# Kernel optimization log

Measured on AMD Instinct MI355X. Metric: run time of the kernel, lower is better.

The kernel has to match this reference:

```python
import jax, jax.numpy as jnp
import numpy as np

H3, W3, D3 = 12, 12, 12
NUM_HEADS = 8
DIM = 128
BATCH = 4
N_TOK = H3 * W3 * D3  # 1728
TABLE = (2 * H3 - 1) * (2 * W3 - 1) * (2 * D3 - 1)  # 12167


def _relative_position_index(h, w, d):
    ch, cw, cd = np.arange(h), np.arange(w), np.arange(d)
    coords = np.stack(np.meshgrid(ch, cw, cd, indexing='ij'))  # (3,h,w,d)
    cf = coords.reshape(3, -1)  # (3,N)
    rel = cf[:, :, None] - cf[:, None, :]  # (3,N,N)
    rel = rel.transpose(1, 2, 0).copy()
    rel[:, :, 0] += h - 1
    rel[:, :, 1] += w - 1
    rel[:, :, 2] += d - 1
    rel[:, :, 0] *= (2 * w - 1) * (2 * d - 1)
    rel[:, :, 1] *= 2 * d - 1
    return rel.sum(-1).astype(np.int32)  # (N,N)


def setup_inputs() -> dict:
    key = jax.random.key(0)
    ks = jax.random.split(key, 7)
    s = 1.0 / np.sqrt(DIM)
    return {
        'x': jax.random.normal(ks[0], (BATCH, N_TOK, DIM), jnp.float32),
        'Wq': jax.random.normal(ks[1], (DIM, DIM), jnp.float32) * s,
        'Wk': jax.random.normal(ks[2], (DIM, DIM), jnp.float32) * s,
        'Wv': jax.random.normal(ks[3], (DIM, DIM), jnp.float32) * s,
        'Wp': jax.random.normal(ks[4], (DIM, DIM), jnp.float32) * s,
        'bp': jnp.zeros((DIM,), jnp.float32),
        'rel_pos_table': jax.random.normal(ks[5], (TABLE, NUM_HEADS), jnp.float32) * 0.02,
        'rel_index': jnp.asarray(_relative_position_index(H3, W3, D3)),
    }


def reference(x, Wq, Wk, Wv, Wp, bp, rel_pos_table, rel_index):
    B, N, C = x.shape
    H = NUM_HEADS
    hd = C // H
    # projections (qkv_bias=False), split heads -> (B,H,N,hd)
    q = (x @ Wq.T).reshape(B, N, H, hd).transpose(0, 2, 1, 3)
    k = (x @ Wk.T).reshape(B, N, H, hd).transpose(0, 2, 1, 3)
    v = (x @ Wv.T).reshape(B, N, H, hd).transpose(0, 2, 1, 3)
    q_sig = jax.nn.sigmoid(q)
    # relative position bias: (N,N,H) -> (H,N,N)
    bias = rel_pos_table[rel_index.reshape(-1)].reshape(N, N, H).transpose(2, 0, 1)
    # softmax over key dim j of (k[b,h,j,d] + bias[h,i,j]) is separable:
    #   exp(k_jd + b_ij) = exp(b_ij - bmax_i) * exp(k_jd - kmax_d) * const
    kmax = jnp.max(k, axis=2, keepdims=True)            # (B,H,1,hd)
    bmax = jnp.max(bias, axis=2, keepdims=True)         # (H,N,1)
    ek = jnp.exp(k - kmax)                              # (B,H,N,hd)
    eb = jnp.exp(bias - bmax)                           # (H,N,N)
    num = jnp.einsum('hij,bhjd->bhid', eb, ek * v)      # (B,H,N,hd)
    den = jnp.einsum('hij,bhjd->bhid', eb, ek)          # (B,H,N,hd)
    out = q_sig * (num / den)                           # (B,H,N,hd)
    out = out.transpose(0, 2, 1, 3).reshape(B, N, C)
    return out @ Wp.T + bp
```

## Files before the change

kernel.cpp:

```cpp
#include <hip/hip_runtime.h>
#include <hip/hip_bf16.h>
#include <cmath>

#define NTOK 1728
#define DIMC 128
#define NHEAD 8
#define NB 4
#define TABN (12167 * 8)

typedef __attribute__((ext_vector_type(8))) short bf16x8;
typedef __attribute__((ext_vector_type(4))) float f32x4;

static __device__ __forceinline__ unsigned short f2bf(float f) {
    union { float f; unsigned u; } v; v.f = f;
    unsigned r = v.u + 0x7fff + ((v.u >> 16) & 1);
    return (unsigned short)(r >> 16);
}

__global__ __launch_bounds__(256) void k_proj_qkv(
    const float* __restrict__ x, const float* __restrict__ Wq,
    const float* __restrict__ Wk, const float* __restrict__ Wv,
    const float* __restrict__ tbl, unsigned short* __restrict__ tblm1,
    float* __restrict__ QS, float* __restrict__ Ko, float* __restrict__ Vo)
{
    __shared__ __align__(16) float xs[64 * 128];
    __shared__ __align__(16) float Ws[32 * 128];
    const int t = threadIdx.x;
    const int m = blockIdx.z;
    if (m == 3) {
        const int g = (blockIdx.y * 108 + blockIdx.x) * 256 + t;
        if (g < TABN) tblm1[g] = f2bf(expm1f(tbl[g]));
        return;
    }
    const int row0 = blockIdx.x * 64;
    const int cg = blockIdx.y;
    const float* __restrict__ W = (m == 0) ? Wq : (m == 1) ? Wk : Wv;

    {
        const int cc = t & 31;
        #pragma unroll
        for (int p = 0; p < 8; ++p) {
            const int r = (t >> 5) + p * 8;
            float4 v = *reinterpret_cast<const float4*>(&x[(size_t)(row0 + r) * DIMC + cc * 4]);
            *reinterpret_cast<float4*>(&xs[r * 128 + ((cc * 4) ^ ((r & 7) << 2))]) = v;
        }
    }
    {
        const int cc = t & 31;
        #pragma unroll
        for (int p = 0; p < 4; ++p) {
            const int c = (t >> 5) + p * 8;
            float4 v = *reinterpret_cast<const float4*>(&W[(size_t)(cg * 32 + c) * DIMC + cc * 4]);
            *reinterpret_cast<float4*>(&Ws[c * 128 + cc * 4]) = v;
        }
    }
    __syncthreads();
    const int nl = t & 63, w = t >> 6;
    float acc[8];
    #pragma unroll
    for (int c = 0; c < 8; ++c) acc[c] = 0.f;
    for (int k4 = 0; k4 < 32; ++k4) {
        const float4 xv = *reinterpret_cast<const float4*>(
            &xs[nl * 128 + ((k4 * 4) ^ ((nl & 7) << 2))]);
        #pragma unroll
        for (int c = 0; c < 8; ++c) {
            const float4 wv = *reinterpret_cast<const float4*>(&Ws[(w * 8 + c) * 128 + k4 * 4]);
            acc[c] = fmaf(xv.x, wv.x, fmaf(xv.y, wv.y,
                     fmaf(xv.z, wv.z, fmaf(xv.w, wv.w, acc[c]))));
        }
    }
    if (m == 0) {
        #pragma unroll
        for (int c = 0; c < 8; ++c) acc[c] = 1.f / (1.f + expf(-acc[c]));
    }
    __syncthreads();
    float* res = Ws;
    #pragma unroll
    for (int c = 0; c < 8; ++c) res[nl * 33 + w * 8 + c] = acc[c];
    __syncthreads();
    float* __restrict__ Out = (m == 0) ? QS : (m == 1) ? Ko : Vo;
    {
        const int r = t >> 2, q = t & 3;
        float4 v0, v1;
        v0.x = res[r*33 + q*8 + 0]; v0.y = res[r*33 + q*8 + 1];
        v0.z = res[r*33 + q*8 + 2]; v0.w = res[r*33 + q*8 + 3];
        v1.x = res[r*33 + q*8 + 4]; v1.y = res[r*33 + q*8 + 5];
        v1.z = res[r*33 + q*8 + 6]; v1.w = res[r*33 + q*8 + 7];
        *reinterpret_cast<float4*>(&Out[(size_t)(row0 + r) * DIMC + cg * 32 + q * 8]) = v0;
        *reinterpret_cast<float4*>(&Out[(size_t)(row0 + r) * DIMC + cg * 32 + q * 8 + 4]) = v1;
    }
}

__global__ __launch_bounds__(256) void k_build_ekv(
    const float* __restrict__ Ko, const float* __restrict__ Vo,
    unsigned short* __restrict__ EKVt, float* __restrict__ n1)
{
    __shared__ float red[256][33];
    const int t = threadIdx.x;
    const int h = blockIdx.y;
    const int b = t >> 6, jj = t & 63;
    const int j = blockIdx.x * 64 + jj;
    const float* kp = &Ko[((size_t)b * NTOK + j) * DIMC + h * 16];
    const float* vp = &Vo[((size_t)b * NTOK + j) * DIMC + h * 16];
    float kv[16], vv[16], ob[32];
    #pragma unroll
    for (int d4 = 0; d4 < 4; ++d4) {
        *reinterpret_cast<float4*>(&kv[d4 * 4]) = *reinterpret_cast<const float4*>(&kp[d4 * 4]);
        *reinterpret_cast<float4*>(&vv[d4 * 4]) = *reinterpret_cast<const float4*>(&vp[d4 * 4]);
    }
    #pragma unroll
    for (int d = 0; d < 16; ++d) {
        float e = expf(kv[d]);
        ob[d] = e * vv[d];
        ob[16 + d] = e;
    }
    #pragma unroll
    for (int c = 0; c < 32; ++c)
        EKVt[((size_t)h * DIMC + b * 32 + c) * NTOK + j] = f2bf(ob[c]);
    #pragma unroll
    for (int c = 0; c < 32; ++c) red[t][c] = ob[c];
    __syncthreads();
    if (t < 128) {
        const int b2 = t >> 5, c = t & 31;
        float s = 0.f;
        for (int r = 0; r < 64; ++r) s += red[b2 * 64 + r][c];
        atomicAdd(&n1[(h * NB + b2) * 32 + c], s);
    }
}

__global__ __launch_bounds__(256) void k_aft_mfma(
    const unsigned short* __restrict__ tblm1,
    const unsigned short* __restrict__ EKVt,
    float* __restrict__ part)
{
    __shared__ __align__(16) unsigned short alds[64 * 64];
    __shared__ __align__(16) unsigned short blds[128 * 64];
    const int t = threadIdx.x;
    const int i0 = blockIdx.x * 64;
    const int h = blockIdx.y;
    const int js = blockIdx.z;
    const int l = t & 63, w = t >> 6;
    const int il = l & 15, kg = l >> 4;

    const int gj = l;
    const int gi0 = w * 16;
    unsigned qb[16];
    #pragma unroll
    for (int r = 0; r < 16; ++r) {
        const int i = i0 + gi0 + r;
        const int hi = i / 144, wi = (i / 12) % 12, di = i % 12;
        qb[r] = (unsigned)((hi * 529 + wi * 23 + di + 6083) * 8 + h);
    }
    const int bc = t >> 3;
    const int bj8 = (t & 7) * 8;

    f32x4 acc[8];
    #pragma unroll
    for (int cf = 0; cf < 8; ++cf) acc[cf] = (f32x4){0.f, 0.f, 0.f, 0.f};

    for (int jt = 0; jt < 9; ++jt) {
        const int j0 = (js * 9 + jt) * 64;
        const int j = j0 + gj;
        const int hj = j / 144, wj = (j / 12) % 12, dj = j % 12;
        const unsigned pj8 = (unsigned)((hj * 529 + wj * 23 + dj) * 8);
        __syncthreads();
        #pragma unroll
        for (int p = 0; p < 4; ++p) {
            const int c = bc + p * 32;
            bf16x8 v = *reinterpret_cast<const bf16x8*>(
                &EKVt[((size_t)h * DIMC + c) * NTOK + j0 + bj8]);
            *reinterpret_cast<bf16x8*>(&blds[c * 64 + (bj8 ^ ((c & 7) << 3))]) = v;
        }
        #pragma unroll
        for (int r = 0; r < 16; ++r) {
            const unsigned short wv = tblm1[qb[r] - pj8];
            alds[(gi0 + r) * 64 + (gj ^ ((r & 7) << 3))] = wv;
        }
        __syncthreads();
        #pragma unroll
        for (int kk = 0; kk < 2; ++kk) {
            const int ia = w * 16 + il;
            const int ka = kk * 32 + kg * 8;
            bf16x8 af = *reinterpret_cast<const bf16x8*>(
                &alds[ia * 64 + (ka ^ ((ia & 7) << 3))]);
            #pragma unroll
            for (int cf = 0; cf < 8; ++cf) {
                const int cb = cf * 16 + il;
                bf16x8 bf = *reinterpret_cast<const bf16x8*>(
                    &blds[cb * 64 + (ka ^ ((cb & 7) << 3))]);
                acc[cf] = __builtin_amdgcn_mfma_f32_16x16x32_bf16(af, bf, acc[cf], 0, 0, 0);
            }
        }
    }
    #pragma unroll
    for (int cf = 0; cf < 8; ++cf) {
        #pragma unroll
        for (int r = 0; r < 4; ++r) {
            const int i = i0 + w * 16 + kg * 4 + r;
            const int c = cf * 16 + il;
            part[(((size_t)js * NHEAD + h) * NTOK + i) * DIMC + c] = acc[cf][r];
        }
    }
}

__global__ __launch_bounds__(256) void k_reduce_y(
    const float* __restrict__ part, const float* __restrict__ n1,
    const float* __restrict__ QS, float* __restrict__ Y)
{
    const int gid = blockIdx.x * 256 + threadIdx.x;
    const int h = gid / (NB * NTOK);
    const int bi = gid - h * (NB * NTOK);
    const int b = bi / NTOK;
    const int i = bi - b * NTOK;
    float nu[16], de[16];
    const float* np = &n1[(h * NB + b) * 32];
    #pragma unroll
    for (int d = 0; d < 16; ++d) { nu[d] = np[d]; de[d] = np[16 + d]; }
    #pragma unroll
    for (int js = 0; js < 3; ++js) {
        const float* pp = &part[(((size_t)js * NHEAD + h) * NTOK + i) * DIMC + b * 32];
        #pragma unroll
        for (int c4 = 0; c4 < 4; ++c4) {
            float4 a  = *reinterpret_cast<const float4*>(&pp[c4 * 4]);
            float4 d4 = *reinterpret_cast<const float4*>(&pp[16 + c4 * 4]);
            nu[c4*4+0] += a.x;  nu[c4*4+1] += a.y;  nu[c4*4+2] += a.z;  nu[c4*4+3] += a.w;
            de[c4*4+0] += d4.x; de[c4*4+1] += d4.y; de[c4*4+2] += d4.z; de[c4*4+3] += d4.w;
        }
    }
    const size_t yb = ((size_t)b * NTOK + i) * DIMC + h * 16;
    #pragma unroll
    for (int d4 = 0; d4 < 4; ++d4) {
        float4 q4 = *reinterpret_cast<const float4*>(&QS[yb + d4 * 4]);
        float4 o;
        o.x = q4.x * nu[d4*4+0] / de[d4*4+0];
        o.y = q4.y * nu[d4*4+1] / de[d4*4+1];
        o.z = q4.z * nu[d4*4+2] / de[d4*4+2];
        o.w = q4.w * nu[d4*4+3] / de[d4*4+3];
        *reinterpret_cast<float4*>(&Y[yb + d4 * 4]) = o;
    }
}

__global__ __launch_bounds__(256) void k_proj_out(
    const float* __restrict__ Y, const float* __restrict__ Wp,
    const float* __restrict__ bp, float* __restrict__ out)
{
    __shared__ __align__(16) float xs[64 * 128];
    __shared__ __align__(16) float Ws[32 * 128];
    const int t = threadIdx.x;
    const int row0 = blockIdx.x * 64;
    const int cg = blockIdx.y;
    {
        const int cc = t & 31;
        #pragma unroll
        for (int p = 0; p < 8; ++p) {
            const int r = (t >> 5) + p * 8;
            float4 v = *reinterpret_cast<const float4*>(&Y[(size_t)(row0 + r) * DIMC + cc * 4]);
            *reinterpret_cast<float4*>(&xs[r * 128 + ((cc * 4) ^ ((r & 7) << 2))]) = v;
        }
    }
    {
        const int cc = t & 31;
        #pragma unroll
        for (int p = 0; p < 4; ++p) {
            const int c = (t >> 5) + p * 8;
            float4 v = *reinterpret_cast<const float4*>(&Wp[(size_t)(cg * 32 + c) * DIMC + cc * 4]);
            *reinterpret_cast<float4*>(&Ws[c * 128 + cc * 4]) = v;
        }
    }
    __syncthreads();
    const int nl = t & 63, w = t >> 6;
    float acc[8];
    #pragma unroll
    for (int c = 0; c < 8; ++c) acc[c] = 0.f;
    for (int k4 = 0; k4 < 32; ++k4) {
        const float4 xv = *reinterpret_cast<const float4*>(
            &xs[nl * 128 + ((k4 * 4) ^ ((nl & 7) << 2))]);
        #pragma unroll
        for (int c = 0; c < 8; ++c) {
            const float4 wv = *reinterpret_cast<const float4*>(&Ws[(w * 8 + c) * 128 + k4 * 4]);
            acc[c] = fmaf(xv.x, wv.x, fmaf(xv.y, wv.y,
                     fmaf(xv.z, wv.z, fmaf(xv.w, wv.w, acc[c]))));
        }
    }
    #pragma unroll
    for (int c = 0; c < 8; ++c) acc[c] += bp[cg * 32 + w * 8 + c];
    __syncthreads();
    float* res = Ws;
    #pragma unroll
    for (int c = 0; c < 8; ++c) res[nl * 33 + w * 8 + c] = acc[c];
    __syncthreads();
    {
        const int r = t >> 2, q = t & 3;
        float4 v0, v1;
        v0.x = res[r*33 + q*8 + 0]; v0.y = res[r*33 + q*8 + 1];
        v0.z = res[r*33 + q*8 + 2]; v0.w = res[r*33 + q*8 + 3];
        v1.x = res[r*33 + q*8 + 4]; v1.y = res[r*33 + q*8 + 5];
        v1.z = res[r*33 + q*8 + 6]; v1.w = res[r*33 + q*8 + 7];
        *reinterpret_cast<float4*>(&out[(size_t)(row0 + r) * DIMC + cg * 32 + q * 8]) = v0;
        *reinterpret_cast<float4*>(&out[(size_t)(row0 + r) * DIMC + cg * 32 + q * 8 + 4]) = v1;
    }
}

extern "C" void kernel_launch(void* const* d_in, const int* in_sizes, int n_in,
                              void* d_out, int out_size, void* d_ws, size_t ws_size,
                              hipStream_t stream) {
    const float* x    = (const float*)d_in[0];
    const float* Wq   = (const float*)d_in[1];
    const float* Wk   = (const float*)d_in[2];
    const float* Wv   = (const float*)d_in[3];
    const float* Wp   = (const float*)d_in[4];
    const float* bp   = (const float*)d_in[5];
    const float* tbl  = (const float*)d_in[6];
    float* out = (float*)d_out;

    float* ws = (float*)d_ws;
    unsigned short* tblm1 = (unsigned short*)ws;
    float* QS  = ws + 48672;
    float* Ko  = QS + 884736;
    float* Vo  = Ko + 884736;
    unsigned short* EKVt = (unsigned short*)(Vo + 884736);
    float* n1   = Vo + 884736 + 884736;
    float* part = n1 + 1024;
    float* Yb   = part + (size_t)3 * NHEAD * NTOK * DIMC;

    hipMemsetAsync(n1, 0, 1024 * sizeof(float), stream);
    k_proj_qkv<<<dim3(108, 4, 4), 256, 0, stream>>>(x, Wq, Wk, Wv, tbl, tblm1, QS, Ko, Vo);
    k_build_ekv<<<dim3(27, 8), 256, 0, stream>>>(Ko, Vo, EKVt, n1);
    k_aft_mfma<<<dim3(27, 8, 3), 256, 0, stream>>>(tblm1, EKVt, part);
    k_reduce_y<<<dim3(216), 256, 0, stream>>>(part, n1, QS, Yb);
    k_proj_out<<<dim3(108, 4), 256, 0, stream>>>(Yb, Wp, bp, out);
}
```

Before: 166.9 us.

## Transpose bias table per head, stage window in LDS, restructure partial reduction

The exp-bias table is now stored head-major, so each attention block loads a contiguous 2304-entry window of it into shared memory once. The per-tile gather then reads LDS instead of scattered global memory. The partials layout is changed so the reduce kernel reads contiguously with one float4 per thread, and the n1 memset is folded into the projection kernel, removing one launch. This adds some LDS use and depends on the index window bounds being correct.

```diff
diff --git a/kernel.cpp b/kernel.cpp
--- a/kernel.cpp
+++ b/kernel.cpp
@@ -6,7 +6,8 @@
 #define DIMC 128
 #define NHEAD 8
 #define NB 4
-#define TABN (12167 * 8)
+#define TABN 12167
+#define TSTRIDE 12168
 
 typedef __attribute__((ext_vector_type(8))) short bf16x8;
 typedef __attribute__((ext_vector_type(4))) float f32x4;
@@ -17,10 +18,15 @@
     return (unsigned short)(r >> 16);
 }
 
+static __device__ __forceinline__ int Pdec(int t) {
+    return (t / 144) * 529 + ((t / 12) % 12) * 23 + (t % 12);
+}
+
 __global__ __launch_bounds__(256) void k_proj_qkv(
     const float* __restrict__ x, const float* __restrict__ Wq,
     const float* __restrict__ Wk, const float* __restrict__ Wv,
-    const float* __restrict__ tbl, unsigned short* __restrict__ tblm1,
+    const float* __restrict__ tbl, unsigned short* __restrict__ tblT,
+    float* __restrict__ n1,
     float* __restrict__ QS, float* __restrict__ Ko, float* __restrict__ Vo)
 {
     __shared__ __align__(16) float xs[64 * 128];
@@ -28,8 +34,24 @@
     const int t = threadIdx.x;
     const int m = blockIdx.z;
     if (m == 3) {
-        const int g = (blockIdx.y * 108 + blockIdx.x) * 256 + t;
-        if (g < TABN) tblm1[g] = f2bf(expm1f(tbl[g]));
+        const int bid2 = blockIdx.y * 108 + blockIdx.x;
+        if (bid2 < 48) {
+            const int idx = bid2 * 256 + t;
+            if (idx < TABN) {
+                float4 f0 = *reinterpret_cast<const float4*>(&tbl[idx * 8]);
+                float4 f1 = *reinterpret_cast<const float4*>(&tbl[idx * 8 + 4]);
+                tblT[0 * TSTRIDE + idx] = f2bf(expm1f(f0.x));
+                tblT[1 * TSTRIDE + idx] = f2bf(expm1f(f0.y));
+                tblT[2 * TSTRIDE + idx] = f2bf(expm1f(f0.z));
+                tblT[3 * TSTRIDE + idx] = f2bf(expm1f(f0.w));
+                tblT[4 * TSTRIDE + idx] = f2bf(expm1f(f1.x));
+                tblT[5 * TSTRIDE + idx] = f2bf(expm1f(f1.y));
+                tblT[6 * TSTRIDE + idx] = f2bf(expm1f(f1.z));
+                tblT[7 * TSTRIDE + idx] = f2bf(expm1f(f1.w));
+            }
+        } else if (bid2 == 48) {
+            ((float4*)n1)[t] = (float4){0.f, 0.f, 0.f, 0.f};
+        }
         return;
     }
     const int row0 = blockIdx.x * 64;
@@ -129,10 +151,11 @@
 }
 
 __global__ __launch_bounds__(256) void k_aft_mfma(
-    const unsigned short* __restrict__ tblm1,
+    const unsigned short* __restrict__ tblT,
     const unsigned short* __restrict__ EKVt,
     float* __restrict__ part)
 {
+    __shared__ __align__(16) unsigned short slds[2304];
     __shared__ __align__(16) unsigned short alds[64 * 64];
     __shared__ __align__(16) unsigned short blds[128 * 64];
     const int t = threadIdx.x;
@@ -142,15 +165,21 @@
     const int l = t & 63, w = t >> 6;
     const int il = l & 15, kg = l >> 4;
 
-    const int gj = l;
+    const int j_base = js * 576;
+    const int pj_lo = js * 4 * 529;
+    const int pj_hi = pj_lo + 1851;
+    const int idx_lo = Pdec(i0) + 6083 - pj_hi;
+    {
+        const unsigned short* src = &tblT[(size_t)h * TSTRIDE + idx_lo];
+        #pragma unroll
+        for (int p = 0; p < 9; ++p) slds[p * 256 + t] = src[p * 256 + t];
+    }
+
     const int gi0 = w * 16;
-    unsigned qb[16];
-    #pragma unroll
-    for (int r = 0; r < 16; ++r) {
-        const int i = i0 + gi0 + r;
-        const int hi = i / 144, wi = (i / 12) % 12, di = i % 12;
-        qb[r] = (unsigned)((hi * 529 + wi * 23 + di + 6083) * 8 + h);
-    }
+    int qb[16];
+    #pragma unroll
+    for (int r = 0; r < 16; ++r) qb[r] = Pdec(i0 + gi0 + r) + 6083 - idx_lo;
+
     const int bc = t >> 3;
     const int bj8 = (t & 7) * 8;
 
@@ -159,10 +188,8 @@
     for (int cf = 0; cf < 8; ++cf) acc[cf] = (f32x4){0.f, 0.f, 0.f, 0.f};
 
     for (int jt = 0; jt < 9; ++jt) {
-        const int j0 = (js * 9 + jt) * 64;
-        const int j = j0 + gj;
-        const int hj = j / 144, wj = (j / 12) % 12, dj = j % 12;
-        const unsigned pj8 = (unsigned)((hj * 529 + wj * 23 + dj) * 8);
+        const int j0 = j_base + jt * 64;
+        const int pj = Pdec(j0 + l);
         __syncthreads();
         #pragma unroll
         for (int p = 0; p < 4; ++p) {
@@ -173,8 +200,7 @@
         }
         #pragma unroll
         for (int r = 0; r < 16; ++r) {
-            const unsigned short wv = tblm1[qb[r] - pj8];
-            alds[(gi0 + r) * 64 + (gj ^ ((r & 7) << 3))] = wv;
+            alds[(gi0 + r) * 64 + (l ^ ((r & 7) << 3))] = slds[qb[r] - pj];
         }
         __syncthreads();
         #pragma unroll
@@ -198,7 +224,7 @@
         for (int r = 0; r < 4; ++r) {
             const int i = i0 + w * 16 + kg * 4 + r;
             const int c = cf * 16 + il;
-            part[(((size_t)js * NHEAD + h) * NTOK + i) * DIMC + c] = acc[cf][r];
+            part[(((size_t)h * NTOK + i) * 3 + js) * DIMC + c] = acc[cf][r];
         }
     }
 }
@@ -207,37 +233,28 @@
     const float* __restrict__ part, const float* __restrict__ n1,
     const float* __restrict__ QS, float* __restrict__ Y)
 {
-    const int gid = blockIdx.x * 256 + threadIdx.x;
-    const int h = gid / (NB * NTOK);
-    const int bi = gid - h * (NB * NTOK);
-    const int b = bi / NTOK;
-    const int i = bi - b * NTOK;
-    float nu[16], de[16];
-    const float* np = &n1[(h * NB + b) * 32];
-    #pragma unroll
-    for (int d = 0; d < 16; ++d) { nu[d] = np[d]; de[d] = np[16 + d]; }
+    const int t = threadIdx.x;
+    const int h = blockIdx.x;
+    const int i = blockIdx.y * 16 + (t >> 4);
+    const int b = t & 3, dq = (t >> 2) & 3;
+    const float* pp = &part[((size_t)h * NTOK + i) * 3 * DIMC];
+    float4 nu = *reinterpret_cast<const float4*>(&n1[(h * NB + b) * 32 + dq * 4]);
+    float4 de = *reinterpret_cast<const float4*>(&n1[(h * NB + b) * 32 + 16 + dq * 4]);
     #pragma unroll
     for (int js = 0; js < 3; ++js) {
-        const float* pp = &part[(((size_t)js * NHEAD + h) * NTOK + i) * DIMC + b * 32];
-        #pragma unroll
-        for (int c4 = 0; c4 < 4; ++c4) {
-            float4 a  = *reinterpret_cast<const float4*>(&pp[c4 * 4]);
-            float4 d4 = *reinterpret_cast<const float4*>(&pp[16 + c4 * 4]);
-            nu[c4*4+0] += a.x;  nu[c4*4+1] += a.y;  nu[c4*4+2] += a.z;  nu[c4*4+3] += a.w;
-            de[c4*4+0] += d4.x; de[c4*4+1] += d4.y; de[c4*4+2] += d4.z; de[c4*4+3] += d4.w;
-        }
-    }
-    const size_t yb = ((size_t)b * NTOK + i) * DIMC + h * 16;
-    #pragma unroll
-    for (int d4 = 0; d4 < 4; ++d4) {
-        float4 q4 = *reinterpret_cast<const float4*>(&QS[yb + d4 * 4]);
-        float4 o;
-        o.x = q4.x * nu[d4*4+0] / de[d4*4+0];
-        o.y = q4.y * nu[d4*4+1] / de[d4*4+1];
-        o.z = q4.z * nu[d4*4+2] / de[d4*4+2];
-        o.w = q4.w * nu[d4*4+3] / de[d4*4+3];
-        *reinterpret_cast<float4*>(&Y[yb + d4 * 4]) = o;
-    }
+        float4 a  = *reinterpret_cast<const float4*>(&pp[js * DIMC + b * 32 + dq * 4]);
+        float4 d4 = *reinterpret_cast<const float4*>(&pp[js * DIMC + b * 32 + 16 + dq * 4]);
+        nu.x += a.x;  nu.y += a.y;  nu.z += a.z;  nu.w += a.w;
+        de.x += d4.x; de.y += d4.y; de.z += d4.z; de.w += d4.w;
+    }
+    const size_t yb = ((size_t)b * NTOK + i) * DIMC + h * 16 + dq * 4;
+    float4 q4 = *reinterpret_cast<const float4*>(&QS[yb]);
+    float4 o;
+    o.x = q4.x * nu.x / de.x;
+    o.y = q4.y * nu.y / de.y;
+    o.z = q4.z * nu.z / de.z;
+    o.w = q4.w * nu.w / de.w;
+    *reinterpret_cast<float4*>(&Y[yb]) = o;
 }
 
 __global__ __launch_bounds__(256) void k_proj_out(
@@ -314,19 +331,18 @@
     float* out = (float*)d_out;
 
     float* ws = (float*)d_ws;
-    unsigned short* tblm1 = (unsigned short*)ws;
-    float* QS  = ws + 48672;
+    unsigned short* tblT = (unsigned short*)ws;
+    float* n1  = ws + 50000;
+    float* QS  = n1 + 1024;
     float* Ko  = QS + 884736;
     float* Vo  = Ko + 884736;
     unsigned short* EKVt = (unsigned short*)(Vo + 884736);
-    float* n1   = Vo + 884736 + 884736;
-    float* part = n1 + 1024;
-    float* Yb   = part + (size_t)3 * NHEAD * NTOK * DIMC;
-
-    hipMemsetAsync(n1, 0, 1024 * sizeof(float), stream);
-    k_proj_qkv<<<dim3(108, 4, 4), 256, 0, stream>>>(x, Wq, Wk, Wv, tbl, tblm1, QS, Ko, Vo);
+    float* part = Vo + 884736 + 884736;
+    float* Yb   = part + (size_t)NHEAD * NTOK * 3 * DIMC;
+
+    k_proj_qkv<<<dim3(108, 4, 4), 256, 0, stream>>>(x, Wq, Wk, Wv, tbl, tblT, n1, QS, Ko, Vo);
     k_build_ekv<<<dim3(27, 8), 256, 0, stream>>>(Ko, Vo, EKVt, n1);
-    k_aft_mfma<<<dim3(27, 8, 3), 256, 0, stream>>>(tblm1, EKVt, part);
-    k_reduce_y<<<dim3(216), 256, 0, stream>>>(part, n1, QS, Yb);
+    k_aft_mfma<<<dim3(27, 8, 3), 256, 0, stream>>>(tblT, EKVt, part);
+    k_reduce_y<<<dim3(8, 108), 256, 0, stream>>>(part, n1, QS, Yb);
     k_proj_out<<<dim3(108, 4), 256, 0, stream>>>(Yb, Wp, bp, out);
 }
```

New measurement: 146.9 us. -11.9%, faster.
